# Kernel tuning notes

Measured on AMD Instinct MI355X. Metric: run time of the kernel, lower is better.

Reference implementation:

```python
import jax, jax.numpy as jnp
import numpy as np

T, N, K = 32, 1024, 15
IN_CH, CONV_CH, HEADS, ODIM = 64, 64, 2, 50
D = CONV_CH // 2  # GRU hidden size (conv_ch // 2)


def setup_inputs():
    ks = jax.random.split(jax.random.key(0), 24)
    x = jax.random.normal(ks[0], (T, N, IN_CH), jnp.float32)
    # fixed-degree adjacency: exactly K distinct non-self sources per (t, target)
    rnd = jax.random.uniform(ks[1], (T, N, N - 1))
    off = jnp.argsort(rnd, axis=-1)[..., :K]            # [T,N,K] in [0, N-2]
    tgt = jnp.arange(N)[None, :, None]
    src = (tgt + 1 + off) % N                           # distinct sources != target
    edge = jnp.zeros((T, N, N), jnp.int32).at[jnp.arange(T)[:, None, None], src, tgt].set(1)

    def lin(k, fi, fo):
        return jax.random.normal(k, (fi, fo), jnp.float32) / float(np.sqrt(fi))

    p, i = {}, 2
    for nm, fi, c in (("g1", IN_CH, CONV_CH), ("g2", CONV_CH, D), ("r1", D, CONV_CH), ("f1", D, CONV_CH)):
        p[nm + "_Wl"] = lin(ks[i], fi, HEADS * c)
        p[nm + "_bl"] = jnp.zeros((HEADS * c,), jnp.float32)
        p[nm + "_Wr"] = lin(ks[i + 1], fi, HEADS * c)
        p[nm + "_br"] = jnp.zeros((HEADS * c,), jnp.float32)
        p[nm + "_att"] = jax.random.normal(ks[i + 2], (HEADS, c), jnp.float32) / float(np.sqrt(c))
        p[nm + "_b"] = jnp.zeros((c,), jnp.float32)
        i += 3
    for nm in ("gru0", "gru1"):
        p[nm + "_Wih"] = lin(ks[i], D, 3 * D).T         # [3D, D], PyTorch layout
        p[nm + "_Whh"] = lin(ks[i + 1], D, 3 * D).T
        p[nm + "_bih"] = jnp.zeros((3 * D,), jnp.float32)
        p[nm + "_bhh"] = jnp.zeros((3 * D,), jnp.float32)
        i += 2
    p["rec2_W"] = lin(ks[i], CONV_CH, IN_CH)
    p["rec2_b"] = jnp.zeros((IN_CH,), jnp.float32)
    p["rec3_W"] = lin(ks[i + 1], IN_CH, ODIM)
    p["rec3_b"] = jnp.zeros((ODIM,), jnp.float32)
    p["fore3_W"] = lin(ks[i + 2], IN_CH, ODIM)
    p["fore3_b"] = jnp.zeros((ODIM,), jnp.float32)
    return {"x": x, "edge": edge, **p}


def _gat(x, srcs, prm):
    # GATv2Conv, concat=False: mean over heads; srcs: [K+1, N] sources per target
    Wl, bl, Wr, br, att, bias = prm
    H, C = att.shape
    gl = (x @ Wl + bl).reshape(-1, H, C)                # source-side lin_l
    gr = (x @ Wr + br).reshape(-1, H, C)                # target-side lin_r
    gsrc = gl[srcs]                                     # [K+1, N, H, C] gather
    e = jax.nn.leaky_relu(gsrc + gr[None], 0.2)
    logits = jnp.einsum('knhc,hc->knh', e, att)
    alpha = jax.nn.softmax(logits, axis=0)              # softmax over neighbors per target
    return jnp.einsum('knh,knhc->nhc', alpha, gsrc).mean(axis=1) + bias


def _gat_t(xs, srcs, prm):
    return jax.vmap(lambda a, s: _gat(a, s, prm))(xs, srcs)


def _gru(xs, Wih, Whh, bih, bhh):
    # PyTorch GRU cell math, zero initial state, seq-first [T, N, D]
    h0 = jnp.zeros((xs.shape[1], Whh.shape[1]), xs.dtype)

    def step(h, xt):
        gi = xt @ Wih.T + bih
        gh = h @ Whh.T + bhh
        ir, iz, inew = jnp.split(gi, 3, axis=-1)
        hr, hz, hn = jnp.split(gh, 3, axis=-1)
        r = jax.nn.sigmoid(ir + hr)
        z = jax.nn.sigmoid(iz + hz)
        n = jnp.tanh(inew + r * hn)
        hnew = (1.0 - z) * n + z * h
        return hnew, hnew

    _, ys = jax.lax.scan(step, h0, xs)
    return ys


def _forward(x, edge, g1, g2, r1, f1, gru0, gru1, rec2_W, rec2_b, rec3_W, rec3_b, fore3_W, fore3_b):
    # recover the K in-edges per target (edge[t, src, tgt] == 1), then append self loops
    srcs = jnp.argsort(-edge, axis=1)[:, :K, :]         # [T, K, N]
    self_idx = jnp.broadcast_to(jnp.arange(N)[None, None, :], (edge.shape[0], 1, N))
    srcs = jnp.concatenate([srcs, self_idx.astype(srcs.dtype)], axis=1)  # [T, K+1, N]

    out = jax.nn.elu(_gat_t(x, srcs, g1))               # dropout is a no-op in eval
    out2 = jax.nn.elu(_gat_t(out, srcs, g2))
    E = _gru(out2, *gru0)
    E = _gru(E, *gru1)

    rec = jax.nn.elu(_gat_t(E[1:], srcs[1:], r1))       # timesteps 1..T-1
    rec = jnp.tanh(rec @ rec2_W + rec2_b)
    recon = rec @ rec3_W + rec3_b

    fc = jax.nn.elu(_gat_t(E[:-1], srcs[:-1], f1))      # timesteps 0..T-2
    fc = jnp.tanh(fc @ rec2_W + rec2_b)                 # original code reuses reconstruct2 here
    forecast = fc @ fore3_W + fore3_b
    return recon, forecast, E


def reference(x, edge, g1_Wl, g1_bl, g1_Wr, g1_br, g1_att, g1_b,
              g2_Wl, g2_bl, g2_Wr, g2_br, g2_att, g2_b,
              r1_Wl, r1_bl, r1_Wr, r1_br, r1_att, r1_b,
              f1_Wl, f1_bl, f1_Wr, f1_br, f1_att, f1_b,
              gru0_Wih, gru0_Whh, gru0_bih, gru0_bhh,
              gru1_Wih, gru1_Whh, gru1_bih, gru1_bhh,
              rec2_W, rec2_b, rec3_W, rec3_b, fore3_W, fore3_b):
    return _forward(x, edge,
                    (g1_Wl, g1_bl, g1_Wr, g1_br, g1_att, g1_b),
                    (g2_Wl, g2_bl, g2_Wr, g2_br, g2_att, g2_b),
                    (r1_Wl, r1_bl, r1_Wr, r1_br, r1_att, r1_b),
                    (f1_Wl, f1_bl, f1_Wr, f1_br, f1_att, f1_b),
                    (gru0_Wih, gru0_Whh, gru0_bih, gru0_bhh),
                    (gru1_Wih, gru1_Whh, gru1_bih, gru1_bhh),
                    rec2_W, rec2_b, rec3_W, rec3_b, fore3_W, fore3_b)
```

## Files before the change

### kernel.cpp

```cpp
#include <hip/hip_runtime.h>
#include <math.h>

static constexpr int Tt = 32;
static constexpr int Nn = 1024;
static constexpr int KN = 16;

template <int M>
__device__ __forceinline__ float lane_xor(float v) {
    if constexpr (M == 1)
        return __int_as_float(__builtin_amdgcn_mov_dpp(__float_as_int(v), 0xB1, 0xF, 0xF, true));
    else if constexpr (M == 2)
        return __int_as_float(__builtin_amdgcn_mov_dpp(__float_as_int(v), 0x4E, 0xF, 0xF, true));
    else
        return __shfl_xor(v, M);
}
__device__ __forceinline__ float bcastlane(float v, int l) {
    return __int_as_float(__builtin_amdgcn_readlane(__float_as_int(v), l));
}
__device__ __forceinline__ constexpr int rev4(int k) {
    return ((k & 1) << 3) | ((k & 2) << 1) | ((k & 4) >> 1) | ((k & 8) >> 3);
}
template <int NV, int M>
__device__ __forceinline__ void fstage(float* p, int lane) {
#pragma unroll
    for (int k2 = 0; k2 < NV / 2; ++k2) {
        float a_ = p[k2], b_ = p[k2 + NV / 2];
        float t_ = (lane & M) ? a_ : b_;
        float r_ = lane_xor<M>(t_);
        p[k2] = ((lane & M) ? b_ : a_) + r_;
    }
}
__device__ __forceinline__ float fold16(float* p, int lane) {
    fstage<16, 1>(p, lane); fstage<8, 2>(p, lane);
    fstage<4, 4>(p, lane);  fstage<2, 8>(p, lane);
    return p[0];
}
__device__ __forceinline__ float rmax16(float x) {
    x = fmaxf(x, lane_xor<1>(x)); x = fmaxf(x, lane_xor<2>(x));
    x = fmaxf(x, lane_xor<4>(x)); x = fmaxf(x, lane_xor<8>(x));
    return x;
}
__device__ __forceinline__ float rsum16(float x) {
    x += lane_xor<1>(x); x += lane_xor<2>(x);
    x += lane_xor<4>(x); x += lane_xor<8>(x);
    return x;
}

__global__ __launch_bounds__(1024) void k_srcs(const int* __restrict__ edge,
                                               int* __restrict__ srcs)
{
    __shared__ int cnt[128];
    const int t    = blockIdx.x >> 3;
    const int tgt0 = (blockIdx.x & 7) << 7;
    const int x = threadIdx.x & 31;
    const int y = threadIdx.x >> 5;
    if (threadIdx.x < 128) cnt[threadIdx.x] = 0;
    __syncthreads();

    const int c0 = 4 * x;
    const int s0 = y * 32;
    const int* e = edge + (size_t)t * Nn * Nn + tgt0 + c0;

    for (int i0 = 0; i0 < 32; i0 += 8) {
        int4 v[8];
#pragma unroll
        for (int j = 0; j < 8; ++j)
            v[j] = *reinterpret_cast<const int4*>(e + (size_t)(s0 + i0 + j) * Nn);
#pragma unroll
        for (int j = 0; j < 8; ++j) {
            const int s = s0 + i0 + j;
            if (v[j].x) { int sl = atomicAdd(&cnt[c0],     1); if (sl < KN - 1) srcs[((size_t)t * Nn + tgt0 + c0)     * KN + sl] = s; }
            if (v[j].y) { int sl = atomicAdd(&cnt[c0 + 1], 1); if (sl < KN - 1) srcs[((size_t)t * Nn + tgt0 + c0 + 1) * KN + sl] = s; }
            if (v[j].z) { int sl = atomicAdd(&cnt[c0 + 2], 1); if (sl < KN - 1) srcs[((size_t)t * Nn + tgt0 + c0 + 2) * KN + sl] = s; }
            if (v[j].w) { int sl = atomicAdd(&cnt[c0 + 3], 1); if (sl < KN - 1) srcs[((size_t)t * Nn + tgt0 + c0 + 3) * KN + sl] = s; }
        }
    }
    if (threadIdx.x < 128)
        srcs[((size_t)t * Nn + tgt0 + threadIdx.x) * KN + (KN - 1)] = tgt0 + threadIdx.x;
}

template <int FI, int FO>
__global__ __launch_bounds__(256) void k_lin2t(
    const float* __restrict__ X,
    const float* __restrict__ Wl, const float* __restrict__ bl,
    const float* __restrict__ Wr, const float* __restrict__ br,
    float* __restrict__ Yl, float* __restrict__ Yr, int rows)
{
    constexpr int HC = FO / 2;
    constexpr int RG = 256 / HC;
    constexpr int R  = 8;
    constexpr int BR = RG * R;
    constexpr int F4 = FI / 4;
    __shared__ float xs[BR][FI];

    const int tid  = threadIdx.x;
    const int c    = tid % HC;
    const int g    = tid / HC;
    const int row0 = blockIdx.x * BR;

#pragma unroll
    for (int idx = tid; idx < BR * F4; idx += 256) {
        int r = idx / F4, q = idx % F4;
        reinterpret_cast<float4*>(&xs[r][0])[q] =
            reinterpret_cast<const float4*>(X + (size_t)(row0 + r) * FI)[q];
    }
    __syncthreads();

    float al0[R], al1[R], ar0[R], ar1[R];
    const float bl0 = bl[c], bl1 = bl[c + HC], br0 = br[c], br1 = br[c + HC];
#pragma unroll
    for (int r = 0; r < R; ++r) { al0[r] = bl0; al1[r] = bl1; ar0[r] = br0; ar1[r] = br1; }

    const int rb = g * R;
#pragma unroll
    for (int i0 = 0; i0 < FI; i0 += 4) {
        float4 xv[R];
#pragma unroll
        for (int r = 0; r < R; ++r)
            xv[r] = *reinterpret_cast<const float4*>(&xs[rb + r][i0]);
#pragma unroll
        for (int j = 0; j < 4; ++j) {
            const float wl0 = Wl[(i0 + j) * FO + c];
            const float wl1 = Wl[(i0 + j) * FO + c + HC];
            const float wr0 = Wr[(i0 + j) * FO + c];
            const float wr1 = Wr[(i0 + j) * FO + c + HC];
#pragma unroll
            for (int r = 0; r < R; ++r) {
                const float xx = (&xv[r].x)[j];
                al0[r] = fmaf(xx, wl0, al0[r]);
                al1[r] = fmaf(xx, wl1, al1[r]);
                ar0[r] = fmaf(xx, wr0, ar0[r]);
                ar1[r] = fmaf(xx, wr1, ar1[r]);
            }
        }
    }
#pragma unroll
    for (int r = 0; r < R; ++r) {
        const size_t ro = (size_t)(row0 + rb + r) * FO;
        reinterpret_cast<float2*>(Yl + ro)[c] = make_float2(al0[r], al1[r]);
        reinterpret_cast<float2*>(Yr + ro)[c] = make_float2(ar0[r], ar1[r]);
    }
}

__global__ __launch_bounds__(256) void k_lin2td(
    const float* __restrict__ E,
    const float* __restrict__ WlA, const float* __restrict__ blA,
    const float* __restrict__ WrA, const float* __restrict__ brA,
    float* __restrict__ YlA, float* __restrict__ YrA,
    const float* __restrict__ WlB, const float* __restrict__ blB,
    const float* __restrict__ WrB, const float* __restrict__ brB,
    float* __restrict__ YlB, float* __restrict__ YrB)
{
    constexpr int FI = 32, FO = 128, HC = 64, R = 8, BR = 32, F4 = FI / 4;
    __shared__ float xs[BR][FI];

    int bid = blockIdx.x;
    const bool second = bid >= 992;
    if (second) bid -= 992;

    const float* X  = second ? E   : (E + (size_t)Nn * FI);
    const float* Wl = second ? WlB : WlA;
    const float* bl = second ? blB : blA;
    const float* Wr = second ? WrB : WrA;
    const float* br = second ? brB : brA;
    float* Yl = second ? YlB : YlA;
    float* Yr = second ? YrB : YrA;

    const int tid  = threadIdx.x;
    const int c    = tid % HC;
    const int g    = tid / HC;
    const int row0 = bid * BR;

#pragma unroll
    for (int idx = tid; idx < BR * F4; idx += 256) {
        int r = idx / F4, q = idx % F4;
        reinterpret_cast<float4*>(&xs[r][0])[q] =
            reinterpret_cast<const float4*>(X + (size_t)(row0 + r) * FI)[q];
    }
    __syncthreads();

    float al0[R], al1[R], ar0[R], ar1[R];
    const float bl0 = bl[c], bl1 = bl[c + HC], br0 = br[c], br1 = br[c + HC];
#pragma unroll
    for (int r = 0; r < R; ++r) { al0[r] = bl0; al1[r] = bl1; ar0[r] = br0; ar1[r] = br1; }

    const int rb = g * R;
#pragma unroll
    for (int i0 = 0; i0 < FI; i0 += 4) {
        float4 xv[R];
#pragma unroll
        for (int r = 0; r < R; ++r)
            xv[r] = *reinterpret_cast<const float4*>(&xs[rb + r][i0]);
#pragma unroll
        for (int j = 0; j < 4; ++j) {
            const float wl0 = Wl[(i0 + j) * FO + c];
            const float wl1 = Wl[(i0 + j) * FO + c + HC];
            const float wr0 = Wr[(i0 + j) * FO + c];
            const float wr1 = Wr[(i0 + j) * FO + c + HC];
#pragma unroll
            for (int r = 0; r < R; ++r) {
                const float xx = (&xv[r].x)[j];
                al0[r] = fmaf(xx, wl0, al0[r]);
                al1[r] = fmaf(xx, wl1, al1[r]);
                ar0[r] = fmaf(xx, wr0, ar0[r]);
                ar1[r] = fmaf(xx, wr1, ar1[r]);
            }
        }
    }
#pragma unroll
    for (int r = 0; r < R; ++r) {
        const size_t ro = (size_t)(row0 + rb + r) * FO;
        reinterpret_cast<float2*>(Yl + ro)[c] = make_float2(al0[r], al1[r]);
        reinterpret_cast<float2*>(Yr + ro)[c] = make_float2(ar0[r], ar1[r]);
    }
}

__global__ __launch_bounds__(192) void k_lin96(
    const float* __restrict__ X, const float* __restrict__ W,
    const float* __restrict__ b, float* __restrict__ Y)
{
    __shared__ float wT[32 * 97];
    __shared__ float xs[16][32];

    const int tid = threadIdx.y * 96 + threadIdx.x;
    const int row0 = blockIdx.x * 16;

    for (int idx = tid; idx < 3072; idx += 192) {
        int c = idx >> 5, i = idx & 31;
        wT[i * 97 + c] = W[idx];
    }
    for (int idx = tid; idx < 128; idx += 192)
        reinterpret_cast<float4*>(xs)[idx] =
            reinterpret_cast<const float4*>(X + (size_t)row0 * 32)[idx];
    __syncthreads();

    const int c  = threadIdx.x;
    const int rb = threadIdx.y * 8;
    float acc[8];
    const float bc = b[c];
#pragma unroll
    for (int r = 0; r < 8; ++r) acc[r] = bc;

#pragma unroll
    for (int i = 0; i < 32; ++i) {
        const float w = wT[i * 97 + c];
#pragma unroll
        for (int r = 0; r < 8; ++r)
            acc[r] = fmaf(xs[rb + r][i], w, acc[r]);
    }
#pragma unroll
    for (int r = 0; r < 8; ++r)
        Y[(size_t)(row0 + rb + r) * 96 + c] = acc[r];
}

__global__ __launch_bounds__(64) void k_gru1(
    const float* __restrict__ gi, const float* __restrict__ Whh,
    const float* __restrict__ bhh, float* __restrict__ E)
{
    const int d    = threadIdx.x & 31;
    const int node = blockIdx.x * 2 + (threadIdx.x >> 5);

    float wr_[32], wz_[32], wn_[32];
#pragma unroll
    for (int q = 0; q < 8; ++q) {
        *reinterpret_cast<float4*>(&wr_[q * 4]) =
            reinterpret_cast<const float4*>(Whh + (size_t)d * 32)[q];
        *reinterpret_cast<float4*>(&wz_[q * 4]) =
            reinterpret_cast<const float4*>(Whh + (size_t)(32 + d) * 32)[q];
        *reinterpret_cast<float4*>(&wn_[q * 4]) =
            reinterpret_cast<const float4*>(Whh + (size_t)(64 + d) * 32)[q];
    }
    const float br_ = bhh[d], bz_ = bhh[32 + d], bn_ = bhh[64 + d];

    size_t base = (size_t)node * 96 + d;
    float gr = gi[base], gz = gi[base + 32], gn = gi[base + 64];

    float h = 0.0f;
    for (int t = 0; t < Tt; ++t) {
        float grn = 0.f, gzn = 0.f, gnn = 0.f;
        if (t < Tt - 1) {
            const size_t nb = ((size_t)(t + 1) * Nn + node) * 96 + d;
            grn = gi[nb]; gzn = gi[nb + 32]; gnn = gi[nb + 64];
        }
        float ar = br_, az = bz_, an = bn_;
#pragma unroll
        for (int i = 0; i < 32; ++i) {
            const float hv = __shfl(h, i, 32);
            ar = fmaf(wr_[i], hv, ar);
            az = fmaf(wz_[i], hv, az);
            an = fmaf(wn_[i], hv, an);
        }
        const float r = __builtin_amdgcn_rcpf(1.0f + expf(-(gr + ar)));
        const float z = __builtin_amdgcn_rcpf(1.0f + expf(-(gz + az)));
        const float nn2 = tanhf(gn + r * an);
        h = (1.0f - z) * nn2 + z * h;
        E[((size_t)t * Nn + node) * 32 + d] = h;
        gr = grn; gz = gzn; gn = gnn;
    }
}

__device__ __forceinline__ float gat64_body(
    const float* __restrict__ gl, const float* __restrict__ gr,
    const int* __restrict__ srcs, const float* __restrict__ att,
    const float* __restrict__ bias, int wave, int lane)
{
    const int t = wave >> 10;
    const int n = wave & (Nn - 1);

    const float2 grl = reinterpret_cast<const float2*>(gr + (size_t)wave * 128)[lane];
    const float a0 = att[lane], a1 = att[64 + lane];

    const int4* sp = reinterpret_cast<const int4*>(srcs + ((size_t)t * Nn + n) * KN);
    const int4 sA = sp[0], sB = sp[1], sC = sp[2], sD = sp[3];
    int s[KN] = {sA.x, sA.y, sA.z, sA.w, sB.x, sB.y, sB.z, sB.w,
                 sC.x, sC.y, sC.z, sC.w, sD.x, sD.y, sD.z, sD.w};

    const float2* glt = reinterpret_cast<const float2*>(gl) + ((size_t)t * Nn * 64);

    float2 g[KN];
    float p0[KN], p1[KN];
#pragma unroll
    for (int k = 0; k < KN; ++k) {
        g[k] = glt[(unsigned)((s[k] << 6) | lane)];
        float e0 = g[k].x + grl.x; e0 = fmaxf(e0, 0.2f * e0);
        float e1 = g[k].y + grl.y; e1 = fmaxf(e1, 0.2f * e1);
        p0[k] = e0 * a0; p1[k] = e1 * a1;
    }
    float lo0 = fold16(p0, lane);
    lo0 += lane_xor<16>(lo0); lo0 += __shfl_xor(lo0, 32);
    float lo1 = fold16(p1, lane);
    lo1 += lane_xor<16>(lo1); lo1 += __shfl_xor(lo1, 32);

    const float m0 = rmax16(lo0), m1 = rmax16(lo1);
    const float e0 = expf(lo0 - m0), e1 = expf(lo1 - m1);
    const float A0 = e0 * __builtin_amdgcn_rcpf(rsum16(e0));
    const float A1 = e1 * __builtin_amdgcn_rcpf(rsum16(e1));

    float acc0 = 0.0f, acc1 = 0.0f;
#pragma unroll
    for (int k = 0; k < KN; ++k) {
        acc0 = fmaf(bcastlane(A0, rev4(k)), g[k].x, acc0);
        acc1 = fmaf(bcastlane(A1, rev4(k)), g[k].y, acc1);
    }
    float res = 0.5f * (acc0 + acc1) + bias[lane];
    return res > 0.0f ? res : expm1f(res);
}

__global__ __launch_bounds__(256, 4) void k_gat64(
    const float* __restrict__ gl, const float* __restrict__ gr,
    const int* __restrict__ srcs, const float* __restrict__ att,
    const float* __restrict__ bias, float* __restrict__ out, int rows)
{
    const int lane = threadIdx.x & 63;
    const int w = threadIdx.x >> 6;
    const int gridB = rows >> 2;
    const int chunk = gridB >> 3;
    const int bid = blockIdx.x;
    const int lb = (bid & 7) * chunk + (bid >> 3);
    const int wave = lb * 4 + w;
    const float res = gat64_body(gl, gr, srcs, att, bias, wave, lane);
    out[(size_t)wave * 64 + lane] = res;
}

__global__ __launch_bounds__(256, 4) void k_gat32(
    const float* __restrict__ gl, const float* __restrict__ gr,
    const int* __restrict__ srcs, const float* __restrict__ att,
    const float* __restrict__ bias, float* __restrict__ out, int waves)
{
    const int lane = threadIdx.x & 63;
    const int w = threadIdx.x >> 6;
    const int gridB = waves >> 2;
    const int chunk = gridB >> 3;
    const int bid = blockIdx.x;
    const int lb = (bid & 7) * chunk + (bid >> 3);
    const int wv = lb * 4 + w;
    const int tgt = 2 * wv + (lane >> 5);
    const int t = tgt >> 10;
    const int n = tgt & (Nn - 1);
    const int c = lane & 31;

    const float2 grl = reinterpret_cast<const float2*>(gr + (size_t)tgt * 64)[c];
    const float a0 = att[c], a1 = att[32 + c];

    const int4* sp = reinterpret_cast<const int4*>(srcs + ((size_t)t * Nn + n) * KN);
    const int4 sA = sp[0], sB = sp[1], sC = sp[2], sD = sp[3];
    int s[KN] = {sA.x, sA.y, sA.z, sA.w, sB.x, sB.y, sB.z, sB.w,
                 sC.x, sC.y, sC.z, sC.w, sD.x, sD.y, sD.z, sD.w};

    const float2* glt = reinterpret_cast<const float2*>(gl) + ((size_t)t * Nn * 32);

    float2 g[KN];
    float p0[KN], p1[KN];
#pragma unroll
    for (int k = 0; k < KN; ++k) {
        g[k] = glt[(unsigned)((s[k] << 5) | c)];
        float e0 = g[k].x + grl.x; e0 = fmaxf(e0, 0.2f * e0);
        float e1 = g[k].y + grl.y; e1 = fmaxf(e1, 0.2f * e1);
        p0[k] = e0 * a0; p1[k] = e1 * a1;
    }
    float lo0 = fold16(p0, lane); lo0 += lane_xor<16>(lo0);
    float lo1 = fold16(p1, lane); lo1 += lane_xor<16>(lo1);

    const float m0 = rmax16(lo0), m1 = rmax16(lo1);
    const float e0 = expf(lo0 - m0), e1 = expf(lo1 - m1);
    const float A0 = e0 * __builtin_amdgcn_rcpf(rsum16(e0));
    const float A1 = e1 * __builtin_amdgcn_rcpf(rsum16(e1));

    const float A0o = __shfl_xor(A0, 32);
    const float A1o = __shfl_xor(A1, 32);
    const bool loHalf = (lane < 32);

    float acc0 = 0.0f, acc1 = 0.0f;
#pragma unroll
    for (int k = 0; k < KN; ++k) {
        const float b0a = bcastlane(A0, rev4(k)), b0b = bcastlane(A0o, rev4(k));
        const float b1a = bcastlane(A1, rev4(k)), b1b = bcastlane(A1o, rev4(k));
        acc0 = fmaf(loHalf ? b0a : b0b, g[k].x, acc0);
        acc1 = fmaf(loHalf ? b1a : b1b, g[k].y, acc1);
    }
    float res = 0.5f * (acc0 + acc1) + bias[c];
    res = res > 0.0f ? res : expm1f(res);
    out[(size_t)tgt * 32 + c] = res;
}

__global__ __launch_bounds__(256) void k_head2(
    const float* __restrict__ inA, const float* __restrict__ W3A,
    const float* __restrict__ b3A, float* __restrict__ outA,
    const float* __restrict__ inB, const float* __restrict__ W3B,
    const float* __restrict__ b3B, float* __restrict__ outB,
    const float* __restrict__ W2, const float* __restrict__ b2)
{
    __shared__ float xs[32][64];
    __shared__ float tmp[32][64];

    int bid = blockIdx.x;
    const bool second = bid >= 992;
    if (second) bid -= 992;

    const float* in  = second ? inB  : inA;
    const float* W3  = second ? W3B  : W3A;
    const float* b3  = second ? b3B  : b3A;
    float*       out = second ? outB : outA;

    const int c = threadIdx.x;
    const int g = threadIdx.y;
    const int tid = g * 64 + c;
    const int row0 = bid * 32;

    for (int idx = tid; idx < 32 * 16; idx += 256) {
        int r = idx >> 4, q = idx & 15;
        reinterpret_cast<float4*>(&xs[r][0])[q] =
            reinterpret_cast<const float4*>(in + (size_t)(row0 + r) * 64)[q];
    }
    __syncthreads();

    const int rb = g * 8;
    float acc[8];
    const float bc = b2[c];
#pragma unroll
    for (int r = 0; r < 8; ++r) acc[r] = bc;
#pragma unroll
    for (int i = 0; i < 64; ++i) {
        const float w2 = W2[i * 64 + c];
#pragma unroll
        for (int r = 0; r < 8; ++r)
            acc[r] = fmaf(xs[rb + r][i], w2, acc[r]);
    }
#pragma unroll
    for (int r = 0; r < 8; ++r) tmp[rb + r][c] = tanhf(acc[r]);

    const int cc = c < 50 ? c : 0;
    float a[8];
    const float b3c = b3[cc];
#pragma unroll
    for (int r = 0; r < 8; ++r) a[r] = b3c;
#pragma unroll
    for (int j = 0; j < 64; ++j) {
        const float w3 = W3[j * 50 + cc];
#pragma unroll
        for (int r = 0; r < 8; ++r)
            a[r] = fmaf(tmp[rb + r][j], w3, a[r]);
    }
    if (c < 50) {
#pragma unroll
        for (int r = 0; r < 8; ++r)
            out[(size_t)(row0 + rb + r) * 50 + c] = a[r];
    }
}

extern "C" void kernel_launch(void* const* d_in, const int* in_sizes, int n_in,
                              void* d_out, int out_size, void* d_ws, size_t ws_size,
                              hipStream_t stream)
{
    const float* x    = (const float*)d_in[0];
    const int*   edge = (const int*)d_in[1];

    const float *g1_Wl = (const float*)d_in[2],  *g1_bl = (const float*)d_in[3];
    const float *g1_Wr = (const float*)d_in[4],  *g1_br = (const float*)d_in[5];
    const float *g1_att= (const float*)d_in[6],  *g1_b  = (const float*)d_in[7];
    const float *g2_Wl = (const float*)d_in[8],  *g2_bl = (const float*)d_in[9];
    const float *g2_Wr = (const float*)d_in[10], *g2_br = (const float*)d_in[11];
    const float *g2_att= (const float*)d_in[12], *g2_b  = (const float*)d_in[13];
    const float *r1_Wl = (const float*)d_in[14], *r1_bl = (const float*)d_in[15];
    const float *r1_Wr = (const float*)d_in[16], *r1_br = (const float*)d_in[17];
    const float *r1_att= (const float*)d_in[18], *r1_b  = (const float*)d_in[19];
    const float *f1_Wl = (const float*)d_in[20], *f1_bl = (const float*)d_in[21];
    const float *f1_Wr = (const float*)d_in[22], *f1_br = (const float*)d_in[23];
    const float *f1_att= (const float*)d_in[24], *f1_b  = (const float*)d_in[25];
    const float *gru0_Wih = (const float*)d_in[26], *gru0_Whh = (const float*)d_in[27];
    const float *gru0_bih = (const float*)d_in[28], *gru0_bhh = (const float*)d_in[29];
    const float *gru1_Wih = (const float*)d_in[30], *gru1_Whh = (const float*)d_in[31];
    const float *gru1_bih = (const float*)d_in[32], *gru1_bhh = (const float*)d_in[33];
    const float *rec2_W = (const float*)d_in[34], *rec2_b = (const float*)d_in[35];
    const float *rec3_W = (const float*)d_in[36], *rec3_b = (const float*)d_in[37];
    const float *fore3_W= (const float*)d_in[38], *fore3_b= (const float*)d_in[39];

    char* ws = (char*)d_ws;
    int*   srcs = (int*)ws;
    float* buf1 = (float*)(ws + (4u << 20));
    float* buf2 = buf1 + (size_t)32768 * 128;
    float* buf3 = buf2 + (size_t)32768 * 128;
    float* buf4 = buf3 + (size_t)32768 * 128;
    float* buf5 = buf4 + (size_t)32768 * 128;
    float* buf6 = buf5 + (size_t)32768 * 64;

    float* recon = (float*)d_out;
    float* fore  = recon + (size_t)31 * 1024 * 50;
    float* E     = fore  + (size_t)31 * 1024 * 50;

    k_srcs<<<Tt * 8, 1024, 0, stream>>>(edge, srcs);

    k_lin2t<64, 128><<<1024, 256, 0, stream>>>(x, g1_Wl, g1_bl, g1_Wr, g1_br, buf1, buf2, 32768);
    k_gat64<<<8192, 256, 0, stream>>>(buf1, buf2, srcs, g1_att, g1_b, buf5, 32768);

    k_lin2t<64, 64><<<512, 256, 0, stream>>>(buf5, g2_Wl, g2_bl, g2_Wr, g2_br, buf1, buf2, 32768);
    k_gat32<<<4096, 256, 0, stream>>>(buf1, buf2, srcs, g2_att, g2_b, buf6, 16384);

    k_lin96<<<2048, dim3(96, 2), 0, stream>>>(buf6, gru0_Wih, gru0_bih, buf1);
    k_gru1<<<512, 64, 0, stream>>>(buf1, gru0_Whh, gru0_bhh, buf5);
    k_lin96<<<2048, dim3(96, 2), 0, stream>>>(buf5, gru1_Wih, gru1_bih, buf2);
    k_gru1<<<512, 64, 0, stream>>>(buf2, gru1_Whh, gru1_bhh, E);

    k_lin2td<<<1984, 256, 0, stream>>>(E,
        r1_Wl, r1_bl, r1_Wr, r1_br, buf1, buf2,
        f1_Wl, f1_bl, f1_Wr, f1_br, buf3, buf4);

    k_gat64<<<7936, 256, 0, stream>>>(buf1, buf2, srcs + (size_t)KN * Nn, r1_att, r1_b, buf5, 31744);
    k_gat64<<<7936, 256, 0, stream>>>(buf3, buf4, srcs, f1_att, f1_b, buf1, 31744);
    k_head2<<<1984, dim3(64, 4), 0, stream>>>(
        buf5, rec3_W, rec3_b, recon,
        buf1, fore3_W, fore3_b, fore,
        rec2_W, rec2_b);

    (void)in_sizes; (void)n_in; (void)out_size; (void)ws_size;
}
```

Measured before the change: 290.2 us.

## Process two GAT64 targets per wave and merge the r1/f1 GAT launches

```diff
diff --git a/kernel.cpp b/kernel.cpp
--- a/kernel.cpp
+++ b/kernel.cpp
@@ -299,16 +299,22 @@
     }
 }
 
-__device__ __forceinline__ float gat64_body(
+__device__ __forceinline__ void gat64_pair_body(
     const float* __restrict__ gl, const float* __restrict__ gr,
     const int* __restrict__ srcs, const float* __restrict__ att,
-    const float* __restrict__ bias, int wave, int lane)
-{
-    const int t = wave >> 10;
-    const int n = wave & (Nn - 1);
-
-    const float2 grl = reinterpret_cast<const float2*>(gr + (size_t)wave * 128)[lane];
-    const float a0 = att[lane], a1 = att[64 + lane];
+    const float* __restrict__ bias, int wv, int lane,
+    float* __restrict__ out)
+{
+    const int tgt = 2 * wv + (lane >> 5);
+    const int t = tgt >> 10;
+    const int n = tgt & (Nn - 1);
+    const int c = lane & 31;
+
+    const float2* grrow = reinterpret_cast<const float2*>(gr) + (size_t)tgt * 64;
+    const float2 grl0 = grrow[c];
+    const float2 grl1 = grrow[32 + c];
+    const float a00 = att[c],      a01 = att[32 + c];
+    const float a10 = att[64 + c], a11 = att[96 + c];
 
     const int4* sp = reinterpret_cast<const int4*>(srcs + ((size_t)t * Nn + n) * KN);
     const int4 sA = sp[0], sB = sp[1], sC = sp[2], sD = sp[3];
@@ -317,49 +323,95 @@
 
     const float2* glt = reinterpret_cast<const float2*>(gl) + ((size_t)t * Nn * 64);
 
-    float2 g[KN];
+    float2 g0[KN], g1[KN];
     float p0[KN], p1[KN];
 #pragma unroll
     for (int k = 0; k < KN; ++k) {
-        g[k] = glt[(unsigned)((s[k] << 6) | lane)];
-        float e0 = g[k].x + grl.x; e0 = fmaxf(e0, 0.2f * e0);
-        float e1 = g[k].y + grl.y; e1 = fmaxf(e1, 0.2f * e1);
-        p0[k] = e0 * a0; p1[k] = e1 * a1;
-    }
-    float lo0 = fold16(p0, lane);
-    lo0 += lane_xor<16>(lo0); lo0 += __shfl_xor(lo0, 32);
-    float lo1 = fold16(p1, lane);
-    lo1 += lane_xor<16>(lo1); lo1 += __shfl_xor(lo1, 32);
+        const unsigned ro = (unsigned)(s[k] << 6);
+        g0[k] = glt[ro | c];
+        g1[k] = glt[ro | (32 + c)];
+        float e00 = g0[k].x + grl0.x; e00 = fmaxf(e00, 0.2f * e00);
+        float e01 = g1[k].x + grl1.x; e01 = fmaxf(e01, 0.2f * e01);
+        float e10 = g0[k].y + grl0.y; e10 = fmaxf(e10, 0.2f * e10);
+        float e11 = g1[k].y + grl1.y; e11 = fmaxf(e11, 0.2f * e11);
+        p0[k] = fmaf(e01, a01, e00 * a00);
+        p1[k] = fmaf(e11, a11, e10 * a10);
+    }
+    float lo0 = fold16(p0, lane); lo0 += lane_xor<16>(lo0);
+    float lo1 = fold16(p1, lane); lo1 += lane_xor<16>(lo1);
 
     const float m0 = rmax16(lo0), m1 = rmax16(lo1);
     const float e0 = expf(lo0 - m0), e1 = expf(lo1 - m1);
     const float A0 = e0 * __builtin_amdgcn_rcpf(rsum16(e0));
     const float A1 = e1 * __builtin_amdgcn_rcpf(rsum16(e1));
 
-    float acc0 = 0.0f, acc1 = 0.0f;
+    const float A0o = __shfl_xor(A0, 32);
+    const float A1o = __shfl_xor(A1, 32);
+    const bool loHalf = (lane < 32);
+
+    float acc00 = 0.0f, acc01 = 0.0f, acc10 = 0.0f, acc11 = 0.0f;
 #pragma unroll
     for (int k = 0; k < KN; ++k) {
-        acc0 = fmaf(bcastlane(A0, rev4(k)), g[k].x, acc0);
-        acc1 = fmaf(bcastlane(A1, rev4(k)), g[k].y, acc1);
-    }
-    float res = 0.5f * (acc0 + acc1) + bias[lane];
-    return res > 0.0f ? res : expm1f(res);
-}
-
-__global__ __launch_bounds__(256, 4) void k_gat64(
+        const float b0a = bcastlane(A0, rev4(k)), b0b = bcastlane(A0o, rev4(k));
+        const float b1a = bcastlane(A1, rev4(k)), b1b = bcastlane(A1o, rev4(k));
+        const float b0 = loHalf ? b0a : b0b;
+        const float b1 = loHalf ? b1a : b1b;
+        acc00 = fmaf(b0, g0[k].x, acc00);
+        acc01 = fmaf(b0, g1[k].x, acc01);
+        acc10 = fmaf(b1, g0[k].y, acc10);
+        acc11 = fmaf(b1, g1[k].y, acc11);
+    }
+    float r0 = 0.5f * (acc00 + acc10) + bias[c];
+    float r1 = 0.5f * (acc01 + acc11) + bias[32 + c];
+    r0 = r0 > 0.0f ? r0 : expm1f(r0);
+    r1 = r1 > 0.0f ? r1 : expm1f(r1);
+    out[(size_t)tgt * 64 + c]      = r0;
+    out[(size_t)tgt * 64 + 32 + c] = r1;
+}
+
+__global__ __launch_bounds__(256, 3) void k_gat64p(
     const float* __restrict__ gl, const float* __restrict__ gr,
     const int* __restrict__ srcs, const float* __restrict__ att,
-    const float* __restrict__ bias, float* __restrict__ out, int rows)
+    const float* __restrict__ bias, float* __restrict__ out, int pairs)
 {
     const int lane = threadIdx.x & 63;
     const int w = threadIdx.x >> 6;
-    const int gridB = rows >> 2;
+    const int gridB = pairs >> 2;
     const int chunk = gridB >> 3;
     const int bid = blockIdx.x;
     const int lb = (bid & 7) * chunk + (bid >> 3);
-    const int wave = lb * 4 + w;
-    const float res = gat64_body(gl, gr, srcs, att, bias, wave, lane);
-    out[(size_t)wave * 64 + lane] = res;
+    const int wv = lb * 4 + w;
+    gat64_pair_body(gl, gr, srcs, att, bias, wv, lane, out);
+}
+
+__global__ __launch_bounds__(256, 3) void k_gat64p2(
+    const float* __restrict__ glA, const float* __restrict__ grA,
+    const int* __restrict__ srcsA, const float* __restrict__ attA,
+    const float* __restrict__ biasA, float* __restrict__ outA,
+    const float* __restrict__ glB, const float* __restrict__ grB,
+    const int* __restrict__ srcsB, const float* __restrict__ attB,
+    const float* __restrict__ biasB, float* __restrict__ outB)
+{
+    constexpr int pairs = (Tt - 1) * Nn / 2;
+    constexpr int gridH = pairs >> 2;
+    constexpr int chunk = gridH >> 3;
+
+    int bid = blockIdx.x;
+    const bool second = bid >= gridH;
+    if (second) bid -= gridH;
+
+    const float* gl   = second ? glB   : glA;
+    const float* gr   = second ? grB   : grA;
+    const int*   srcs = second ? srcsB : srcsA;
+    const float* att  = second ? attB  : attA;
+    const float* bias = second ? biasB : biasA;
+    float*       out  = second ? outB  : outA;
+
+    const int lane = threadIdx.x & 63;
+    const int w = threadIdx.x >> 6;
+    const int lb = (bid & 7) * chunk + (bid >> 3);
+    const int wv = lb * 4 + w;
+    gat64_pair_body(gl, gr, srcs, att, bias, wv, lane, out);
 }
 
 __global__ __launch_bounds__(256, 4) void k_gat32(
@@ -531,7 +583,7 @@
     k_srcs<<<Tt * 8, 1024, 0, stream>>>(edge, srcs);
 
     k_lin2t<64, 128><<<1024, 256, 0, stream>>>(x, g1_Wl, g1_bl, g1_Wr, g1_br, buf1, buf2, 32768);
-    k_gat64<<<8192, 256, 0, stream>>>(buf1, buf2, srcs, g1_att, g1_b, buf5, 32768);
+    k_gat64p<<<4096, 256, 0, stream>>>(buf1, buf2, srcs, g1_att, g1_b, buf5, 16384);
 
     k_lin2t<64, 64><<<512, 256, 0, stream>>>(buf5, g2_Wl, g2_bl, g2_Wr, g2_br, buf1, buf2, 32768);
     k_gat32<<<4096, 256, 0, stream>>>(buf1, buf2, srcs, g2_att, g2_b, buf6, 16384);
@@ -545,11 +597,12 @@
         r1_Wl, r1_bl, r1_Wr, r1_br, buf1, buf2,
         f1_Wl, f1_bl, f1_Wr, f1_br, buf3, buf4);
 
-    k_gat64<<<7936, 256, 0, stream>>>(buf1, buf2, srcs + (size_t)KN * Nn, r1_att, r1_b, buf5, 31744);
-    k_gat64<<<7936, 256, 0, stream>>>(buf3, buf4, srcs, f1_att, f1_b, buf1, 31744);
+    k_gat64p2<<<7936, 256, 0, stream>>>(
+        buf1, buf2, srcs + (size_t)KN * Nn, r1_att, r1_b, buf5,
+        buf3, buf4, srcs,                   f1_att, f1_b, buf6);
     k_head2<<<1984, dim3(64, 4), 0, stream>>>(
         buf5, rec3_W, rec3_b, recon,
-        buf1, fore3_W, fore3_b, fore,
+        buf6, fore3_W, fore3_b, fore,
         rec2_W, rec2_b);
 
     (void)in_sizes; (void)n_in; (void)out_size; (void)ws_size;
```

New measurement: 283.6 us. 1.02x faster.
